# Kernel tuning notes

Hardware: AMD Instinct MI355X
Metric: run time of the kernel (lower is better)

Reference implementation:

```python
import jax, jax.numpy as jnp
import numpy as np

N = 262144
LOC_ENC_LEN = 60
NUM_WEIGHTS = 8
INDIM = 32
OUTDIM = 32
HIDDEN = 32
NEG_SLOPE = 0.01  # nn.LeakyReLU default


def _linear_init(key, fan_in, fan_out):
    # torch nn.Linear default: U(-1/sqrt(fan_in), 1/sqrt(fan_in))
    kw, kb = jax.random.split(key)
    bound = 1.0 / np.sqrt(fan_in)
    w = jax.random.uniform(kw, (fan_in, fan_out), jnp.float32, -bound, bound)
    b = jax.random.uniform(kb, (fan_out,), jnp.float32, -bound, bound)
    return w, b


def setup_inputs() -> dict:
    key = jax.random.key(0)
    ks = jax.random.split(key, 10)
    rel_loc_feat = jax.random.normal(ks[0], (N, LOC_ENC_LEN), jnp.float32)
    feat = jax.random.normal(ks[1], (N, INDIM), jnp.float32)
    dims = [LOC_ENC_LEN, HIDDEN, HIDDEN, HIDDEN, HIDDEN, HIDDEN, NUM_WEIGHTS]
    params = {}
    for i in range(6):
        w, b = _linear_init(ks[2 + i], dims[i], dims[i + 1])
        params[f'sn_w{i}'] = w
        params[f'sn_b{i}'] = b
    # weights_bank: kaiming_normal on [num_weights, indim*outdim] -> std = sqrt(2/fan_in), fan_in = indim*outdim
    std = np.sqrt(2.0 / (INDIM * OUTDIM))
    params['bank'] = jax.random.normal(ks[9], (NUM_WEIGHTS, INDIM * OUTDIM), jnp.float32) * std
    return {'rel_loc_feat': rel_loc_feat, 'feat': feat, **params}


def _score_net(x, ws, bs):
    # 5 Linear+LeakyReLU blocks, then final Linear (no activation)
    for i in range(5):
        x = x @ ws[i] + bs[i]
        x = jnp.where(x >= 0, x, NEG_SLOPE * x)
    return x @ ws[5] + bs[5]


def reference(rel_loc_feat, feat,
              sn_w0, sn_b0, sn_w1, sn_b1, sn_w2, sn_b2,
              sn_w3, sn_b3, sn_w4, sn_b4, sn_w5, sn_b5, bank):
    ws = [sn_w0, sn_w1, sn_w2, sn_w3, sn_w4, sn_w5]
    bs = [sn_b0, sn_b1, sn_b2, sn_b3, sn_b4, sn_b5]
    logits = _score_net(rel_loc_feat, ws, bs)          # [N, num_weights]
    coeff = jax.nn.softmax(logits, axis=-1)            # [N, num_weights]
    # per-point weight matrix: [N, indim*outdim] -> [N, indim, outdim]
    weights = (coeff @ bank).reshape(coeff.shape[0], INDIM, OUTDIM)
    # per-point matmul: feat[:, None] @ weights -> squeeze
    out = jnp.einsum('ni,nio->no', feat, weights)      # [N, outdim]
    return out
```

## Files before the change

### kernel.cpp

```cpp
#include <hip/hip_runtime.h>
#include <stdint.h>


typedef __attribute__((ext_vector_type(8))) __bf16 bf16x8;
typedef __attribute__((ext_vector_type(2))) __bf16 bf16x2;
typedef __attribute__((ext_vector_type(4))) float f32x4;

union FragU { uint32_t u[4]; bf16x8 v; uint4 q; };

__device__ __forceinline__ unsigned short f2bf(float f) {
    union { float f; uint32_t i; } v; v.f = f;
    return (unsigned short)((v.i + 0x7FFFu + ((v.i >> 16) & 1u)) >> 16);
}
__device__ __forceinline__ float bf2f(uint32_t u16) {
    union { uint32_t i; float f; } v; v.i = u16 << 16; return v.f;
}
__device__ __forceinline__ uint32_t pk2(float x, float y) {
    union { bf16x2 h; uint32_t u; } c;
    c.h[0] = (__bf16)x; c.h[1] = (__bf16)y;
    return c.u;
}
__device__ __forceinline__ bf16x8 pack8(float a, float b, float c, float d,
                                        float e, float f, float g, float h) {
    bf16x8 v;
    v[0] = (__bf16)a; v[1] = (__bf16)b; v[2] = (__bf16)c; v[3] = (__bf16)d;
    v[4] = (__bf16)e; v[5] = (__bf16)f; v[6] = (__bf16)g; v[7] = (__bf16)h;
    return v;
}
__device__ __forceinline__ int permK(int k) {
    return 4 * (k >> 3) + (k & 3) + 16 * ((k >> 2) & 1);
}
__device__ __forceinline__ f32x4 MF(bf16x8 a, bf16x8 b, f32x4 c) {
    return __builtin_amdgcn_mfma_f32_16x16x32_bf16(a, b, c, 0, 0, 0);
}


struct WPf { const float* p[13]; };

__global__ void pc_prep(WPf wp, uint32_t* __restrict__ ws) {
    int idx = blockIdx.x * blockDim.x + threadIdx.x;
    if (idx >= 10240) return;
    if (idx < 7424) {
        int layer, t, chunk = 0, lane, d; const float* w; bool perm;
        int r = idx;
        if (r < 1024) { chunk = r >> 9; r &= 511; t = r >> 8; r &= 255; lane = r >> 2; d = r & 3;
                        layer = 0; w = wp.p[0]; perm = false; }
        else if (r < 3072) { r -= 1024; layer = 1 + (r >> 9); r &= 511; t = r >> 8; r &= 255;
                             lane = r >> 2; d = r & 3; w = wp.p[2 * layer]; perm = true; }
        else if (r < 3328) { r -= 3072; layer = 5; t = 0; lane = r >> 2; d = r & 3;
                             w = wp.p[10]; perm = true; }
        else { r -= 3328; int bk = r >> 9; r &= 511; t = r >> 8; r &= 255; lane = r >> 2; d = r & 3;
               layer = -1; w = wp.p[12] + bk * 1024; perm = false; }
        int gq = lane >> 4, m = t * 16 + (lane & 15);
        uint32_t o = 0;
        #pragma unroll
        for (int e = 0; e < 2; ++e) {
            int kf = 8 * gq + 2 * d + e;
            float v = 0.f;
            if (layer == -1) {
                v = w[kf * 32 + m];
            } else {
                int ks = perm ? permK(kf) : (chunk * 32 + kf);
                if (layer == 0)      { if (ks < 60) v = w[ks * 32 + m]; }
                else if (layer == 5) { if (m < 8)   v = w[ks * 8 + m]; }
                else                 v = w[ks * 32 + m];
            }
            o |= ((uint32_t)f2bf(v)) << (16 * e);
        }
        ws[idx] = o;
    } else if (idx < 9984) {
        int r = idx - 7424; int L = r >> 9; r &= 511; int t = r >> 8; r &= 255;
        int lane = r >> 2, rr = r & 3;
        ((float*)ws)[idx] = wp.p[2 * L + 1][t * 16 + 4 * (lane >> 4) + rr];
    } else {
        int r = idx - 9984; int lane = r >> 2, rr = r & 3;
        int m = 4 * (lane >> 4) + rr;
        ((float*)ws)[idx] = (m < 8) ? wp.p[11][m] : 0.f;
    }
}

#define IT 2

#define CO 10240

__global__ __launch_bounds__(256, 3) void pc_main(
    const float* __restrict__ rel, const float* __restrict__ feat,
    const uint32_t* __restrict__ wsu, float* __restrict__ out)
{
    __shared__ __align__(16) uint32_t W[11264];
    {
        uint4* s4 = (uint4*)W;
        const uint4* g4 = (const uint4*)wsu;
        #pragma unroll
        for (int i = 0; i < 10; ++i) {
            int idx = threadIdx.x + 256 * i;
            int src = (idx < 832) ? idx
                    : (idx < 1536) ? idx + 1024
                    : idx - 704;
            s4[idx] = g4[src];
        }
    }
    __syncthreads();

    const int lane = threadIdx.x & 63;
    const int wv = threadIdx.x >> 6;
    const int g = lane >> 4;
    const int n16 = lane & 15;
    const size_t pt0 = (size_t)(blockIdx.x * 4 + wv) * (32 * IT);
    const int pbase = wv * (32 * IT);

    #define LDF(off) ({ FragU _f; _f.q = ((const uint4*)(W + (off)))[lane]; _f.v; })
    #define LDB(off) ({ float4 _b = ((const float4*)(W + (off)))[lane]; \
                        (f32x4){_b.x, _b.y, _b.z, _b.w}; })

    for (int it = 0; it < IT; ++it) {
        const size_t nA = pt0 + (size_t)it * 32 + n16;

        bf16x8 c0[2], c1[2];
        #pragma unroll
        for (int q = 0; q < 2; ++q) {
            const float* rrow = rel + (nA + 16 * q) * 60;
            float4 ra = *(const float4*)(rrow + 8 * g);
            float4 rb = *(const float4*)(rrow + 8 * g + 4);
            float4 rc = *(const float4*)(rrow + 32 + 8 * g);
            float4 rd = make_float4(0.f, 0.f, 0.f, 0.f);
            if (g < 3) rd = *(const float4*)(rrow + 36 + 8 * g);
            c0[q] = pack8(ra.x, ra.y, ra.z, ra.w, rb.x, rb.y, rb.z, rb.w);
            c1[q] = pack8(rc.x, rc.y, rc.z, rc.w, rd.x, rd.y, rd.z, rd.w);
        }

        f32x4 t0[2], t1[2];
        {
            f32x4 ba = LDB(3328), bb = LDB(3328 + 256);
            bf16x8 w00 = LDF(0), w01 = LDF(256), w10 = LDF(512), w11 = LDF(768);
            #pragma unroll
            for (int q = 0; q < 2; ++q) {
                t0[q] = MF(w00, c0[q], ba);    t1[q] = MF(w01, c0[q], bb);
                t0[q] = MF(w10, c1[q], t0[q]); t1[q] = MF(w11, c1[q], t1[q]);
            }
        }

        #pragma unroll
        for (int L = 0; L < 4; ++L) {
            bf16x8 wa = LDF(1024 + L * 512), wb = LDF(1024 + L * 512 + 256);
            f32x4 ba = LDB(3328 + (L + 1) * 512), bb = LDB(3328 + (L + 1) * 512 + 256);
            #pragma unroll
            for (int q = 0; q < 2; ++q) {
                #pragma unroll
                for (int r = 0; r < 4; ++r) {
                    t0[q][r] = fmaxf(t0[q][r], 0.01f * t0[q][r]);
                    t1[q][r] = fmaxf(t1[q][r], 0.01f * t1[q][r]);
                }
                bf16x8 bx = pack8(t0[q][0], t0[q][1], t0[q][2], t0[q][3],
                                  t1[q][0], t1[q][1], t1[q][2], t1[q][3]);
                t0[q] = MF(wa, bx, ba);
                t1[q] = MF(wb, bx, bb);
            }
        }

        {
            bf16x8 w5 = LDF(3072);
            f32x4 b5 = LDB(5888);
            #pragma unroll
            for (int q = 0; q < 2; ++q) {
                #pragma unroll
                for (int r = 0; r < 4; ++r) {
                    t0[q][r] = fmaxf(t0[q][r], 0.01f * t0[q][r]);
                    t1[q][r] = fmaxf(t1[q][r], 0.01f * t1[q][r]);
                }
                bf16x8 bx = pack8(t0[q][0], t0[q][1], t0[q][2], t0[q][3],
                                  t1[q][0], t1[q][1], t1[q][2], t1[q][3]);
                t0[q] = MF(w5, bx, b5);
            }
        }

        #pragma unroll
        for (int q = 0; q < 2; ++q) {
            float m4 = fmaxf(fmaxf(t0[q][0], t0[q][1]), fmaxf(t0[q][2], t0[q][3]));
            float m8 = fmaxf(m4, __shfl_xor(m4, 16, 64));
            float e0 = __expf(t0[q][0] - m8), e1 = __expf(t0[q][1] - m8);
            float e2 = __expf(t0[q][2] - m8), e3 = __expf(t0[q][3] - m8);
            float s4 = e0 + e1 + e2 + e3;
            float s8 = s4 + __shfl_xor(s4, 16, 64);
            float inv = 1.0f / s8;
            uint32_t p01 = pk2(e0 * inv, e1 * inv);
            uint32_t p23 = pk2(e2 * inv, e3 * inv);
            if (g < 2) {
                int p = pbase + it * 32 + q * 16 + n16;
                *(uint2*)(W + CO + p * 4 + 2 * g) = make_uint2(p01, p23);
            }
        }
    }

    for (int it = 0; it < IT; ++it) {
        const size_t nA = pt0 + (size_t)it * 32 + n16;
        const int p0 = pbase + it * 32 + n16;

        uint4 cp[2];
        #pragma unroll
        for (int q = 0; q < 2; ++q)
            cp[q] = *(const uint4*)(W + CO + (p0 + 16 * q) * 4);

        bf16x8 bfr[2];
        #pragma unroll
        for (int q = 0; q < 2; ++q) {
            const float* frow = feat + (nA + 16 * q) * 32 + 8 * g;
            float4 fa = *(const float4*)frow;
            float4 fb = *(const float4*)(frow + 4);
            bfr[q] = pack8(fa.x, fa.y, fa.z, fa.w, fb.x, fb.y, fb.z, fb.w);
        }

        float cw[2][8];
        #pragma unroll
        for (int q = 0; q < 2; ++q) {
            cw[q][0] = bf2f(cp[q].x & 0xffff); cw[q][1] = bf2f(cp[q].x >> 16);
            cw[q][2] = bf2f(cp[q].y & 0xffff); cw[q][3] = bf2f(cp[q].y >> 16);
            cw[q][4] = bf2f(cp[q].z & 0xffff); cw[q][5] = bf2f(cp[q].z >> 16);
            cw[q][6] = bf2f(cp[q].w & 0xffff); cw[q][7] = bf2f(cp[q].w >> 16);
        }

        f32x4 o0[2], o1[2];
        #pragma unroll
        for (int q = 0; q < 2; ++q) {
            o0[q] = (f32x4){0.f, 0.f, 0.f, 0.f};
            o1[q] = (f32x4){0.f, 0.f, 0.f, 0.f};
        }
        #pragma unroll
        for (int k = 0; k < 8; ++k) {
            bf16x8 wk0 = LDF(6144 + k * 512), wk1 = LDF(6144 + k * 512 + 256);
            #pragma unroll
            for (int q = 0; q < 2; ++q) {
                f32x4 z = {0.f, 0.f, 0.f, 0.f};
                f32x4 u0 = MF(wk0, bfr[q], z);
                f32x4 u1 = MF(wk1, bfr[q], z);
                #pragma unroll
                for (int r = 0; r < 4; ++r) {
                    o0[q][r] += cw[q][k] * u0[r];
                    o1[q][r] += cw[q][k] * u1[r];
                }
            }
        }

        #pragma unroll
        for (int q = 0; q < 2; ++q) {
            float* orow = out + (nA + 16 * q) * 32;
            *(float4*)(orow + 4 * g)      = make_float4(o0[q][0], o0[q][1], o0[q][2], o0[q][3]);
            *(float4*)(orow + 16 + 4 * g) = make_float4(o1[q][0], o1[q][1], o1[q][2], o1[q][3]);
        }
    }
    #undef LDF
    #undef LDB
}

extern "C" void kernel_launch(void* const* d_in, const int* in_sizes, int n_in,
                              void* d_out, int out_size, void* d_ws, size_t ws_size,
                              hipStream_t stream)
{
    const float* rel = (const float*)d_in[0];
    const float* feat = (const float*)d_in[1];
    WPf wp;
    for (int i = 0; i < 13; ++i) wp.p[i] = (const float*)d_in[2 + i];
    uint32_t* ws = (uint32_t*)d_ws;
    float* out = (float*)d_out;

    const int npts = in_sizes[0] / 60;
    const int nblocks = npts / (32 * IT * 4);

    hipLaunchKernelGGL(pc_prep, dim3(40), dim3(256), 0, stream, wp, ws);
    hipLaunchKernelGGL(pc_main, dim3(nblocks), dim3(256), 0, stream, rel, feat, ws, out);
}
```

Baseline: 161.5 us.

## Prefetch rel/feat rows before weight staging and drop per-wave iteration loop

Each wave now handles one 32-point chunk instead of two, so twice as many blocks are launched and the coefficient scratch in shared memory shrinks. All global loads of rel and feat for the block are issued before the weight copy into shared memory and the barrier, so their latency overlaps the weight staging. In exchange, each block amortizes its weight staging over half as many points, and the held float4 registers raise register pressure.

```diff
diff --git a/kernel.cpp b/kernel.cpp
--- a/kernel.cpp
+++ b/kernel.cpp
@@ -79,7 +79,6 @@
     }
 }
 
-#define IT 2
 
 #define CO 10240
 
@@ -87,7 +86,28 @@
     const float* __restrict__ rel, const float* __restrict__ feat,
     const uint32_t* __restrict__ wsu, float* __restrict__ out)
 {
-    __shared__ __align__(16) uint32_t W[11264];
+    __shared__ __align__(16) uint32_t W[10752];
+
+    const int lane = threadIdx.x & 63;
+    const int wv = threadIdx.x >> 6;
+    const int g = lane >> 4;
+    const int n16 = lane & 15;
+    const size_t nA = (size_t)blockIdx.x * 128 + wv * 32 + n16;
+
+    float4 ra[2], rb[2], rc[2], rd[2], fa[2], fb[2];
+    #pragma unroll
+    for (int q = 0; q < 2; ++q) {
+        const float* rrow = rel + (nA + 16 * q) * 60;
+        ra[q] = *(const float4*)(rrow + 8 * g);
+        rb[q] = *(const float4*)(rrow + 8 * g + 4);
+        rc[q] = *(const float4*)(rrow + 32 + 8 * g);
+        rd[q] = make_float4(0.f, 0.f, 0.f, 0.f);
+        if (g < 3) rd[q] = *(const float4*)(rrow + 36 + 8 * g);
+        const float* frow = feat + (nA + 16 * q) * 32 + 8 * g;
+        fa[q] = *(const float4*)frow;
+        fb[q] = *(const float4*)(frow + 4);
+    }
+
     {
         uint4* s4 = (uint4*)W;
         const uint4* g4 = (const uint4*)wsu;
@@ -102,31 +122,18 @@
     }
     __syncthreads();
 
-    const int lane = threadIdx.x & 63;
-    const int wv = threadIdx.x >> 6;
-    const int g = lane >> 4;
-    const int n16 = lane & 15;
-    const size_t pt0 = (size_t)(blockIdx.x * 4 + wv) * (32 * IT);
-    const int pbase = wv * (32 * IT);
-
     #define LDF(off) ({ FragU _f; _f.q = ((const uint4*)(W + (off)))[lane]; _f.v; })
     #define LDB(off) ({ float4 _b = ((const float4*)(W + (off)))[lane]; \
                         (f32x4){_b.x, _b.y, _b.z, _b.w}; })
 
-    for (int it = 0; it < IT; ++it) {
-        const size_t nA = pt0 + (size_t)it * 32 + n16;
-
+    {
         bf16x8 c0[2], c1[2];
         #pragma unroll
         for (int q = 0; q < 2; ++q) {
-            const float* rrow = rel + (nA + 16 * q) * 60;
-            float4 ra = *(const float4*)(rrow + 8 * g);
-            float4 rb = *(const float4*)(rrow + 8 * g + 4);
-            float4 rc = *(const float4*)(rrow + 32 + 8 * g);
-            float4 rd = make_float4(0.f, 0.f, 0.f, 0.f);
-            if (g < 3) rd = *(const float4*)(rrow + 36 + 8 * g);
-            c0[q] = pack8(ra.x, ra.y, ra.z, ra.w, rb.x, rb.y, rb.z, rb.w);
-            c1[q] = pack8(rc.x, rc.y, rc.z, rc.w, rd.x, rd.y, rd.z, rd.w);
+            c0[q] = pack8(ra[q].x, ra[q].y, ra[q].z, ra[q].w,
+                          rb[q].x, rb[q].y, rb[q].z, rb[q].w);
+            c1[q] = pack8(rc[q].x, rc[q].y, rc[q].z, rc[q].w,
+                          rd[q].x, rd[q].y, rd[q].z, rd[q].w);
         }
 
         f32x4 t0[2], t1[2];
@@ -186,29 +193,23 @@
             uint32_t p01 = pk2(e0 * inv, e1 * inv);
             uint32_t p23 = pk2(e2 * inv, e3 * inv);
             if (g < 2) {
-                int p = pbase + it * 32 + q * 16 + n16;
+                int p = wv * 32 + q * 16 + n16;
                 *(uint2*)(W + CO + p * 4 + 2 * g) = make_uint2(p01, p23);
             }
         }
     }
 
-    for (int it = 0; it < IT; ++it) {
-        const size_t nA = pt0 + (size_t)it * 32 + n16;
-        const int p0 = pbase + it * 32 + n16;
-
+    {
         uint4 cp[2];
         #pragma unroll
         for (int q = 0; q < 2; ++q)
-            cp[q] = *(const uint4*)(W + CO + (p0 + 16 * q) * 4);
+            cp[q] = *(const uint4*)(W + CO + (wv * 32 + q * 16 + n16) * 4);
 
         bf16x8 bfr[2];
         #pragma unroll
-        for (int q = 0; q < 2; ++q) {
-            const float* frow = feat + (nA + 16 * q) * 32 + 8 * g;
-            float4 fa = *(const float4*)frow;
-            float4 fb = *(const float4*)(frow + 4);
-            bfr[q] = pack8(fa.x, fa.y, fa.z, fa.w, fb.x, fb.y, fb.z, fb.w);
-        }
+        for (int q = 0; q < 2; ++q)
+            bfr[q] = pack8(fa[q].x, fa[q].y, fa[q].z, fa[q].w,
+                           fb[q].x, fb[q].y, fb[q].z, fb[q].w);
 
         float cw[2][8];
         #pragma unroll
@@ -264,7 +265,7 @@
     float* out = (float*)d_out;
 
     const int npts = in_sizes[0] / 60;
-    const int nblocks = npts / (32 * IT * 4);
+    const int nblocks = npts / 128;
 
     hipLaunchKernelGGL(pc_prep, dim3(40), dim3(256), 0, stream, wp, ws);
     hipLaunchKernelGGL(pc_main, dim3(nblocks), dim3(256), 0, stream, rel, feat, ws, out);
```

New measurement: 160.5 us. Within noise of the previous version (-0.6%).
